# Kernel tuning notes

Measured on AMD Instinct MI355X. Metric: run time of the kernel, lower is better.

## Reference

```python
import jax, jax.numpy as jnp
import numpy as np
jax.config.update("jax_enable_x64", True)

NUM_EMBEDDINGS = 1_000_000
EMBEDDING_DIM = 64
COMPRESSION = 1.0 / 64.0
WEIGHT_SIZE = int(NUM_EMBEDDINGS * EMBEDDING_DIM * COMPRESSION)  # 1,000,000
# Hash constants from the hashed_embedding_bag CUDA extension (dlrm_ssm)
HASH_A = 9824516537
HASH_B = 57857966300227
HASH_P = 117130198221199


def setup_inputs() -> dict:
    key = jax.random.key(0)
    k1, k2 = jax.random.split(key)
    indices = jax.random.randint(k1, (16384, 50), 0, NUM_EMBEDDINGS, dtype=jnp.int64)
    # init: uniform in [-sqrt(1/num_embeddings), sqrt(1/num_embeddings)]
    bound = float(np.sqrt(1.0 / NUM_EMBEDDINGS))
    hashed_weight = jax.random.uniform(
        k2, (WEIGHT_SIZE,), dtype=jnp.float32, minval=-bound, maxval=bound
    )
    return {"hashed_weight": hashed_weight, "indices": indices}


def reference(hashed_weight, indices):
    # 2D indices -> mini-batch of fixed-length bags, mode='sum'
    B, L = indices.shape
    flat = indices.reshape(-1).astype(jnp.int64)  # [B*L]
    d = jnp.arange(EMBEDDING_DIM, dtype=jnp.int64)  # [E]
    # hash each (index, dim) pair into the compressed weight array
    hidx = ((flat[:, None] * HASH_A + d[None, :] * HASH_B) % HASH_P) % WEIGHT_SIZE  # [B*L, E]
    vals = hashed_weight[hidx]  # [B*L, E] gather
    out = vals.reshape(B, L, EMBEDDING_DIM).sum(axis=1)  # per-bag sum -> [B, E]
    return out
```

## Files before the change

kernel.cpp:

```cpp
#include <hip/hip_runtime.h>
#include <stdint.h>


#define BAG_LEN 50
#define EMB_DIM 64
#define WEIGHT_SIZE 1000000ULL
#define HASH_A 9824516537ULL
#define HASH_B 57857966300227ULL
#define HASH_P 117130198221199ULL

__global__ __launch_bounds__(256) void heb_kernel(
    const float* __restrict__ w,
    const int* __restrict__ idx,
    float* __restrict__ out,
    int num_bags)
{
    const int lane = threadIdx.x & 63;
    const int wid  = threadIdx.x >> 6;
    const int bag  = blockIdx.x * 4 + wid;
    if (bag >= num_bags) return;

    const uint64_t hb = ((uint64_t)lane * HASH_B) % HASH_P;

    const int* bag_idx = idx + bag * BAG_LEN;

    float acc = 0.0f;
#pragma unroll
    for (int l = 0; l < BAG_LEN; ++l) {
        const uint64_t i  = (uint64_t)(uint32_t)bag_idx[l];
        uint64_t t = (i * HASH_A) % HASH_P;
        t += hb;
        if (t >= HASH_P) t -= HASH_P;
        const uint32_t h = (uint32_t)(t % WEIGHT_SIZE);
        acc += w[h];
    }

    out[bag * EMB_DIM + lane] = acc;
}

extern "C" void kernel_launch(void* const* d_in, const int* in_sizes, int n_in,
                              void* d_out, int out_size, void* d_ws, size_t ws_size,
                              hipStream_t stream) {
    const float* w   = (const float*)d_in[0];
    const int*   idx = (const int*)d_in[1];
    float*       out = (float*)d_out;

    const int num_bags = out_size / EMB_DIM;
    const int bags_per_block = 4;
    const int grid = (num_bags + bags_per_block - 1) / bags_per_block;

    heb_kernel<<<grid, 256, 0, stream>>>(w, idx, out, num_bags);
}
```

Before: 209.9 us.

## Hoist per-index hash modulo to wave-uniform scalar path and batch gathers

Splits the hash so the expensive 64-bit modulo of index*A is computed once per bag element. The index is wave-uniform once bag goes through readfirstlane, so that modulo can run on the scalar path. Each lane then combines the result with a precomputed per-lane (hb mod W) using 32-bit adds and a wraparound correction constant, which removes the per-lane 64-bit mod. Gathers are issued in groups of ten with two accumulators to expose more memory-level parallelism, and launch bounds are tightened for occupancy. The float summation order changes slightly.

```diff
diff --git a/kernel.cpp b/kernel.cpp
--- a/kernel.cpp
+++ b/kernel.cpp
@@ -4,12 +4,13 @@
 
 #define BAG_LEN 50
 #define EMB_DIM 64
-#define WEIGHT_SIZE 1000000ULL
+#define WEIGHT_SIZE 1000000u
 #define HASH_A 9824516537ULL
 #define HASH_B 57857966300227ULL
 #define HASH_P 117130198221199ULL
+#define W_MINUS_PMODW 778801u
 
-__global__ __launch_bounds__(256) void heb_kernel(
+__global__ __launch_bounds__(256, 8) void heb_kernel(
     const float* __restrict__ w,
     const int* __restrict__ idx,
     float* __restrict__ out,
@@ -17,25 +18,41 @@
 {
     const int lane = threadIdx.x & 63;
     const int wid  = threadIdx.x >> 6;
-    const int bag  = blockIdx.x * 4 + wid;
+    int bag = blockIdx.x * 4 + wid;
+    bag = __builtin_amdgcn_readfirstlane(bag);
     if (bag >= num_bags) return;
 
-    const uint64_t hb = ((uint64_t)lane * HASH_B) % HASH_P;
+    const uint64_t hb     = ((uint64_t)lane * HASH_B) % HASH_P;
+    const uint32_t hb_mod = (uint32_t)(hb % (uint64_t)WEIGHT_SIZE);
 
     const int* bag_idx = idx + bag * BAG_LEN;
 
-    float acc = 0.0f;
+    float acc0 = 0.f, acc1 = 0.f;
+
 #pragma unroll
-    for (int l = 0; l < BAG_LEN; ++l) {
-        const uint64_t i  = (uint64_t)(uint32_t)bag_idx[l];
-        uint64_t t = (i * HASH_A) % HASH_P;
-        t += hb;
-        if (t >= HASH_P) t -= HASH_P;
-        const uint32_t h = (uint32_t)(t % WEIGHT_SIZE);
-        acc += w[h];
+    for (int l0 = 0; l0 < BAG_LEN; l0 += 10) {
+        uint32_t off[10];
+#pragma unroll
+        for (int j = 0; j < 10; ++j) {
+            const uint32_t i  = (uint32_t)bag_idx[l0 + j];
+            const uint64_t mA = ((uint64_t)i * HASH_A) % HASH_P;
+            const uint32_t aS = (uint32_t)(mA % (uint64_t)WEIGHT_SIZE);
+            const uint64_t Pm = HASH_P - mA;
+
+            uint32_t r = aS + hb_mod;
+            if (hb >= Pm) r += W_MINUS_PMODW;
+            if (r >= 2u * WEIGHT_SIZE) r -= 2u * WEIGHT_SIZE;
+            if (r >= WEIGHT_SIZE)      r -= WEIGHT_SIZE;
+            off[j] = r;
+        }
+        float v[10];
+#pragma unroll
+        for (int j = 0; j < 10; ++j) v[j] = w[off[j]];
+#pragma unroll
+        for (int j = 0; j < 10; ++j) { if (j & 1) acc1 += v[j]; else acc0 += v[j]; }
     }
 
-    out[bag * EMB_DIM + lane] = acc;
+    out[bag * EMB_DIM + lane] = acc0 + acc1;
 }
 
 extern "C" void kernel_launch(void* const* d_in, const int* in_sizes, int n_in,
```

Result: no change. 207.1 us (-1.3%).
